# Optimization experiments

Hardware: AMD Instinct MI355X
Metric: run time of the kernel (lower is better)

Reference implementation:

```python
import jax, jax.numpy as jnp
import numpy as np

SPARSITY = 0.5


def get_subnet(s, sparsity):
    # edge-popup GetSubnet: binary mask keeping top (1-sparsity) fraction by value,
    # straight-through gradient (identity) in backward.
    flat = s.ravel()
    j = int(sparsity * flat.size)
    idx = jnp.argsort(flat)  # ascending
    mask = jnp.zeros_like(flat).at[idx[j:]].set(1.0).reshape(s.shape)
    return s + jax.lax.stop_gradient(mask - s)


def setup_inputs() -> dict:
    key = jax.random.key(0)
    k1, k2, k3, k4, k5 = jax.random.split(key, 5)
    B, F, R, O = 4096, 2048, 8, 2048
    return {
        "x": jax.random.normal(k1, (B, F), dtype=jnp.float32),
        "weight1": jax.random.normal(k2, (R, F), dtype=jnp.float32),
        "weight2": jax.random.normal(k3, (O, F * R), dtype=jnp.float32),
        "scores1": jax.random.normal(k4, (R, F), dtype=jnp.float32),
        "scores2": jax.random.normal(k5, (O, F * R), dtype=jnp.float32),
    }


def reference(x, weight1, weight2, scores1, scores2):
    B = x.shape[0]
    # masked weight1, broadcast-multiply repeated input
    w1 = weight1 * get_subnet(jnp.abs(scores1), SPARSITY)        # [R, F]
    h = x[:, None, :] * w1[None, :, :]                           # [B, R, F]
    h = jax.nn.relu(h)
    # permute(0,2,1).reshape -> feature-major flattening [B, F*R]
    h = jnp.transpose(h, (0, 2, 1)).reshape(B, -1)
    # masked weight2, dense GEMM
    w2 = weight2 * get_subnet(jnp.abs(scores2), SPARSITY)        # [O, F*R]
    return h @ w2.T                                              # [B, O]
```

## Files before the change

### kernel.cpp

```cpp
#include <hip/hip_runtime.h>
#include <stdint.h>

#define B_ 4096
#define F_ 2048
#define R_ 8
#define O_ 2048
#define N2 (O_ * F_ * R_)
#define N1 (R_ * F_)
#define K2SEL ((uint32_t)(N2 / 2))
#define K1SEL ((uint32_t)(N1 / 2))
#define TIE_CAP 8192


__device__ __forceinline__ uint32_t fkey(float s) {
    return __float_as_uint(fabsf(s));
}
__device__ __forceinline__ ushort f2bf(float f) {
    uint32_t u = __float_as_uint(f);
    return (ushort)((u + 0x7FFFu + ((u >> 16) & 1u)) >> 16);
}
__device__ __forceinline__ float bf2f(ushort h) {
    return __uint_as_float(((uint32_t)h) << 16);
}

__global__ void init_kernel(uint32_t* w) {
    int t = threadIdx.x;
    for (int i = t; i < 2048; i += 256) w[64 + i] = 0;
    if (t == 0) {
        w[0] = 0; w[1] = K2SEL;
        w[2] = 0; w[3] = K1SEL;
        w[4] = 0; w[5] = 0;
    }
}

__global__ void hist_kernel(const float* __restrict__ s, int n,
                            const uint32_t* __restrict__ state,
                            uint32_t* __restrict__ hist, int pass) {
    __shared__ uint32_t h[256];
    for (int i = threadIdx.x; i < 256; i += blockDim.x) h[i] = 0;
    __syncthreads();

    uint32_t prefix = state[0];
    int shift_pref = 32 - 8 * pass;
    int shift_bin  = 24 - 8 * pass;

    int stride = gridDim.x * blockDim.x;
    int i0 = blockIdx.x * blockDim.x + threadIdx.x;
    const float4* s4 = reinterpret_cast<const float4*>(s);
    int n4 = n >> 2;
    for (int i = i0; i < n4; i += stride) {
        float4 v = s4[i];
        uint32_t b[4] = { fkey(v.x), fkey(v.y), fkey(v.z), fkey(v.w) };
        if (pass == 0) {
            #pragma unroll
            for (int e = 0; e < 4; ++e) atomicAdd(&h[b[e] >> 24], 1u);
        } else {
            #pragma unroll
            for (int e = 0; e < 4; ++e)
                if ((b[e] >> shift_pref) == prefix)
                    atomicAdd(&h[(b[e] >> shift_bin) & 255u], 1u);
        }
    }
    __syncthreads();
    for (int i = threadIdx.x; i < 256; i += blockDim.x)
        if (h[i]) atomicAdd(&hist[i], h[i]);
}

__global__ void scan_kernel(uint32_t* state, const uint32_t* hist) {
    if (threadIdx.x == 0 && blockIdx.x == 0) {
        uint32_t K = state[1];
        uint32_t prefix = state[0];
        uint32_t cum = 0;
        for (int b = 255; b >= 0; --b) {
            uint32_t hb = hist[b];
            if (cum + hb >= K) {
                state[0] = (prefix << 8) | (uint32_t)b;
                state[1] = K - cum;
                break;
            }
            cum += hb;
        }
    }
}

__global__ void tie_kernel(const float* __restrict__ s, int n,
                           const uint32_t* __restrict__ state,
                           uint32_t* __restrict__ count, uint32_t* __restrict__ list) {
    uint32_t target = state[0];
    int stride = gridDim.x * blockDim.x;
    int i0 = blockIdx.x * blockDim.x + threadIdx.x;
    const float4* s4 = reinterpret_cast<const float4*>(s);
    int n4 = n >> 2;
    for (int i = i0; i < n4; i += stride) {
        float4 v = s4[i];
        uint32_t b[4] = { fkey(v.x), fkey(v.y), fkey(v.z), fkey(v.w) };
        #pragma unroll
        for (int e = 0; e < 4; ++e) {
            if (b[e] == target) {
                uint32_t p = atomicAdd(count, 1u);
                if (p < TIE_CAP) list[p] = (uint32_t)(4 * i + e);
            }
        }
    }
}

__global__ void cutoff_kernel(const uint32_t* __restrict__ count,
                              const uint32_t* __restrict__ list,
                              const uint32_t* __restrict__ state,
                              uint32_t* __restrict__ T, int n) {
    __shared__ uint32_t cnt;
    uint32_t c = *count; if (c > TIE_CAP) c = TIE_CAP;
    uint32_t n1 = state[1];
    uint32_t lo = 0, hi = (uint32_t)(n - 1);
    while (lo < hi) {
        uint32_t mid = lo + (hi - lo + 1) / 2;
        if (threadIdx.x == 0) cnt = 0;
        __syncthreads();
        uint32_t local = 0;
        for (uint32_t i = threadIdx.x; i < c; i += blockDim.x)
            if (list[i] >= mid) local++;
        if (local) atomicAdd(&cnt, local);
        __syncthreads();
        uint32_t cv = cnt;
        __syncthreads();
        if (cv >= n1) lo = mid; else hi = mid - 1;
    }
    if (threadIdx.x == 0) { T[0] = lo; T[1] = state[0]; }
}

__global__ void w1t_kernel(const float* __restrict__ w1, const float* __restrict__ s1,
                           const uint32_t* __restrict__ T1,
                           float* __restrict__ w1pt, float* __restrict__ w1nt) {
    int t = blockIdx.x * blockDim.x + threadIdx.x;
    if (t >= N1) return;
    uint32_t tb = T1[1], tc = T1[0];
    int r = t / F_, f = t - r * F_;
    uint32_t kb = fkey(s1[t]);
    bool m = (kb > tb) || (kb == tb && (uint32_t)t >= tc);
    float v = m ? w1[t] : 0.0f;
    w1pt[f * R_ + r] = fmaxf(v, 0.0f);
    w1nt[f * R_ + r] = fminf(v, 0.0f);
}

__global__ void xsplit_kernel(const float* __restrict__ x,
                              ushort* __restrict__ ph, ushort* __restrict__ pl,
                              ushort* __restrict__ nh, ushort* __restrict__ nl) {
    int t = blockIdx.x * blockDim.x + threadIdx.x;
    float4 v = reinterpret_cast<const float4*>(x)[t];
    float vv[4] = { v.x, v.y, v.z, v.w };
    ushort oph[4], opl[4], onh[4], onl[4];
    #pragma unroll
    for (int e = 0; e < 4; ++e) {
        float p = fmaxf(vv[e], 0.f), n = fminf(vv[e], 0.f);
        ushort h1 = f2bf(p); oph[e] = h1; opl[e] = f2bf(p - bf2f(h1));
        ushort h2 = f2bf(n); onh[e] = h2; onl[e] = f2bf(n - bf2f(h2));
    }
    *reinterpret_cast<ushort4*>(&ph[t * 4]) = make_ushort4(oph[0], oph[1], oph[2], oph[3]);
    *reinterpret_cast<ushort4*>(&pl[t * 4]) = make_ushort4(opl[0], opl[1], opl[2], opl[3]);
    *reinterpret_cast<ushort4*>(&nh[t * 4]) = make_ushort4(onh[0], onh[1], onh[2], onh[3]);
    *reinterpret_cast<ushort4*>(&nl[t * 4]) = make_ushort4(onl[0], onl[1], onl[2], onl[3]);
}

__global__ void wbuild_kernel(const float* __restrict__ w2, const float* __restrict__ s2,
                              const uint32_t* __restrict__ T2,
                              const float* __restrict__ w1pt, const float* __restrict__ w1nt,
                              ushort* __restrict__ bph, ushort* __restrict__ bpl,
                              ushort* __restrict__ bnh, ushort* __restrict__ bnl) {
    int t = blockIdx.x * blockDim.x + threadIdx.x;
    int f = t & (F_ - 1);
    uint32_t tb = T2[1], tc = T2[0];
    int base = (t >> 11) * (F_ * R_) + f * R_;

    float4 wa = *reinterpret_cast<const float4*>(w2 + base);
    float4 wb = *reinterpret_cast<const float4*>(w2 + base + 4);
    float4 sa = *reinterpret_cast<const float4*>(s2 + base);
    float4 sb = *reinterpret_cast<const float4*>(s2 + base + 4);
    float4 pa = *reinterpret_cast<const float4*>(w1pt + f * R_);
    float4 pb = *reinterpret_cast<const float4*>(w1pt + f * R_ + 4);
    float4 na = *reinterpret_cast<const float4*>(w1nt + f * R_);
    float4 nb = *reinterpret_cast<const float4*>(w1nt + f * R_ + 4);

    float wv[8] = { wa.x, wa.y, wa.z, wa.w, wb.x, wb.y, wb.z, wb.w };
    float sv[8] = { sa.x, sa.y, sa.z, sa.w, sb.x, sb.y, sb.z, sb.w };
    float pv[8] = { pa.x, pa.y, pa.z, pa.w, pb.x, pb.y, pb.z, pb.w };
    float nv[8] = { na.x, na.y, na.z, na.w, nb.x, nb.y, nb.z, nb.w };

    float accp = 0.f, accn = 0.f;
    #pragma unroll
    for (int r = 0; r < 8; ++r) {
        uint32_t kb = fkey(sv[r]);
        bool m = (kb > tb) || (kb == tb && (uint32_t)(base + r) >= tc);
        float wm = m ? wv[r] : 0.0f;
        accp = fmaf(pv[r], wm, accp);
        accn = fmaf(nv[r], wm, accn);
    }
    ushort h1 = f2bf(accp); bph[t] = h1; bpl[t] = f2bf(accp - bf2f(h1));
    ushort h2 = f2bf(accn); bnh[t] = h2; bnl[t] = f2bf(accn - bf2f(h2));
}

typedef __attribute__((ext_vector_type(8))) short bf16x8;
typedef __attribute__((ext_vector_type(4))) float f32x4;

__device__ __forceinline__ void gload16(const void* g, void* l) {
    __builtin_amdgcn_global_load_lds((const __attribute__((address_space(1))) void*)g,
                                     (__attribute__((address_space(3))) void*)l, 16, 0, 0);
}

__global__ __launch_bounds__(256) void mfma_gemm(
    const ushort* __restrict__ aph, const ushort* __restrict__ apl,
    const ushort* __restrict__ anh, const ushort* __restrict__ anl,
    const ushort* __restrict__ bph, const ushort* __restrict__ bpl,
    const ushort* __restrict__ bnh, const ushort* __restrict__ bnl,
    float* __restrict__ out) {
    __shared__ ushort lds[4][128][32];

    const int tid  = threadIdx.x;
    const int wid  = tid >> 6;
    const int lane = tid & 63;
    const int brow = blockIdx.y * 128;
    const int bcol = blockIdx.x * 128;
    const int wr = (wid >> 1) * 64;
    const int wc = (wid & 1) * 64;

    f32x4 acc[4][4] = {};

    const int srow = lane >> 2;
    const int scol = (lane & 3) * 8;

    #pragma unroll 1
    for (int plane = 0; plane < 2; ++plane) {
        const ushort* tsrc =
            (wid == 0) ? (plane ? anh : aph) :
            (wid == 1) ? (plane ? anl : apl) :
            (wid == 2) ? (plane ? bnh : bph) :
                         (plane ? bnl : bpl);
        const int rowbase = (wid < 2) ? brow : bcol;

        #pragma unroll 1
        for (int k0 = 0; k0 < F_; k0 += 32) {
            #pragma unroll
            for (int t = 0; t < 8; ++t) {
                const ushort* g = tsrc + (size_t)(rowbase + t * 16 + srow) * F_ + k0 + scol;
                gload16(g, (void*)&lds[wid][t * 16][0]);
            }
            __syncthreads();

            bf16x8 ah[4], al[4], bh[4], bl[4];
            const int fr = lane & 15;
            const int kc = (lane >> 4) * 8;
            #pragma unroll
            for (int i = 0; i < 4; ++i) {
                ah[i] = *(const bf16x8*)&lds[0][wr + i * 16 + fr][kc];
                al[i] = *(const bf16x8*)&lds[1][wr + i * 16 + fr][kc];
                bh[i] = *(const bf16x8*)&lds[2][wc + i * 16 + fr][kc];
                bl[i] = *(const bf16x8*)&lds[3][wc + i * 16 + fr][kc];
            }
            #pragma unroll
            for (int i = 0; i < 4; ++i)
                #pragma unroll
                for (int j = 0; j < 4; ++j) {
                    acc[i][j] = __builtin_amdgcn_mfma_f32_16x16x32_bf16(ah[i], bh[j], acc[i][j], 0, 0, 0);
                    acc[i][j] = __builtin_amdgcn_mfma_f32_16x16x32_bf16(ah[i], bl[j], acc[i][j], 0, 0, 0);
                    acc[i][j] = __builtin_amdgcn_mfma_f32_16x16x32_bf16(al[i], bh[j], acc[i][j], 0, 0, 0);
                }
            __syncthreads();
        }
    }

    #pragma unroll
    for (int i = 0; i < 4; ++i) {
        int orow0 = brow + wr + i * 16 + (lane >> 4) * 4;
        #pragma unroll
        for (int j = 0; j < 4; ++j) {
            int ocol = bcol + wc + j * 16 + (lane & 15);
            #pragma unroll
            for (int q = 0; q < 4; ++q)
                out[(size_t)(orow0 + q) * O_ + ocol] = acc[i][j][q];
        }
    }
}

extern "C" void kernel_launch(void* const* d_in, const int* in_sizes, int n_in,
                              void* d_out, int out_size, void* d_ws, size_t ws_size,
                              hipStream_t stream) {
    const float* x  = (const float*)d_in[0];
    const float* w1 = (const float*)d_in[1];
    const float* w2 = (const float*)d_in[2];
    const float* s1 = (const float*)d_in[3];
    const float* s2 = (const float*)d_in[4];
    float* out = (float*)d_out;

    uint32_t* w = (uint32_t*)d_ws;
    uint32_t* state2 = w + 0;
    uint32_t* state1 = w + 2;
    uint32_t* cnt2 = w + 4;
    uint32_t* cnt1 = w + 5;
    uint32_t* T2 = w + 6;
    uint32_t* T1 = w + 8;
    uint32_t* hist2 = w + 64;
    uint32_t* hist1 = w + 1088;
    uint32_t* tie2 = w + 2112;
    uint32_t* tie1 = w + 2112 + TIE_CAP;

    float* w1pt = (float*)((char*)d_ws + 131072);
    float* w1nt = w1pt + N1;

    char* base = (char*)d_ws + 262144;
    ushort* aph = (ushort*)(base);
    ushort* apl = aph + (size_t)B_ * F_;
    ushort* anh = apl + (size_t)B_ * F_;
    ushort* anl = anh + (size_t)B_ * F_;
    ushort* bph = anl + (size_t)B_ * F_;
    ushort* bpl = bph + (size_t)O_ * F_;
    ushort* bnh = bpl + (size_t)O_ * F_;
    ushort* bnl = bnh + (size_t)O_ * F_;

    init_kernel<<<1, 256, 0, stream>>>(w);

    xsplit_kernel<<<(B_ * F_ / 4) / 256, 256, 0, stream>>>(x, aph, apl, anh, anl);

    for (int p = 0; p < 4; ++p) {
        hist_kernel<<<2048, 256, 0, stream>>>(s2, N2, state2, hist2 + p * 256, p);
        scan_kernel<<<1, 1, 0, stream>>>(state2, hist2 + p * 256);
    }
    tie_kernel<<<2048, 256, 0, stream>>>(s2, N2, state2, cnt2, tie2);
    cutoff_kernel<<<1, 256, 0, stream>>>(cnt2, tie2, state2, T2, N2);

    for (int p = 0; p < 4; ++p) {
        hist_kernel<<<64, 256, 0, stream>>>(s1, N1, state1, hist1 + p * 256, p);
        scan_kernel<<<1, 1, 0, stream>>>(state1, hist1 + p * 256);
    }
    tie_kernel<<<64, 256, 0, stream>>>(s1, N1, state1, cnt1, tie1);
    cutoff_kernel<<<1, 256, 0, stream>>>(cnt1, tie1, state1, T1, N1);

    w1t_kernel<<<N1 / 256, 256, 0, stream>>>(w1, s1, T1, w1pt, w1nt);

    wbuild_kernel<<<(O_ * F_) / 256, 256, 0, stream>>>(w2, s2, T2, w1pt, w1nt,
                                                       bph, bpl, bnh, bnl);

    mfma_gemm<<<dim3(O_ / 128, B_ / 128), 256, 0, stream>>>(
        aph, apl, anh, anl, bph, bpl, bnh, bnl, out);
}
```

Baseline: 886.8 us.

## Replace four-pass radix select with 16-bit histogram plus candidate compaction

The median-threshold selection over the 33M-element scores2 drops from four 8-bit histogram passes plus a tie pass to one pass building a 16-bit global histogram, replicated 16 ways to spread atomic contention. A second pass compacts candidates that share the chosen 16-bit prefix, and a single block finishes the remaining bits and tie-breaking from that list. The small scores1 selection is fused into one single-block kernel that works in shared memory and also writes the transposed w1 halves. This cuts full reads of scores2 from five to two and removes many small launches, at the cost of heavy global atomics on 1M bins and a fixed candidate cap that could overflow on skewed inputs.

Result: slower. 3.073 ms (+246.6%).

```diff
diff --git a/kernel.cpp b/kernel.cpp
--- a/kernel.cpp
+++ b/kernel.cpp
@@ -9,7 +9,8 @@
 #define N1 (R_ * F_)
 #define K2SEL ((uint32_t)(N2 / 2))
 #define K1SEL ((uint32_t)(N1 / 2))
-#define TIE_CAP 8192
+#define CAND_CAP (512 * 1024)
+#define TIE_CAP2 4096
 
 
 __device__ __forceinline__ uint32_t fkey(float s) {
@@ -23,123 +24,208 @@
     return __uint_as_float(((uint32_t)h) << 16);
 }
 
-__global__ void init_kernel(uint32_t* w) {
+__global__ void init_kernel(uint32_t* st, uint32_t* h16) {
+    int i0 = blockIdx.x * blockDim.x + threadIdx.x;
+    int stride = gridDim.x * blockDim.x;
+    for (int i = i0; i < 16 * 65536; i += stride) h16[i] = 0;
+    if (i0 == 0) st[4] = 0;
+}
+
+__global__ void hist16_kernel(const float* __restrict__ s, uint32_t* __restrict__ h16) {
+    int stride = gridDim.x * blockDim.x;
+    int i0 = blockIdx.x * blockDim.x + threadIdx.x;
+    uint32_t rep = ((uint32_t)blockIdx.x & 15u) << 16;
+    const float4* s4 = reinterpret_cast<const float4*>(s);
+    for (int i = i0; i < N2 / 4; i += stride) {
+        float4 v = s4[i];
+        atomicAdd(&h16[rep | (fkey(v.x) >> 16)], 1u);
+        atomicAdd(&h16[rep | (fkey(v.y) >> 16)], 1u);
+        atomicAdd(&h16[rep | (fkey(v.z) >> 16)], 1u);
+        atomicAdd(&h16[rep | (fkey(v.w) >> 16)], 1u);
+    }
+}
+
+__global__ void scan16_kernel(uint32_t* __restrict__ h16, uint32_t* __restrict__ st) {
+    __shared__ uint32_t csum[256];
     int t = threadIdx.x;
-    for (int i = t; i < 2048; i += 256) w[64 + i] = 0;
+    int base = t * 256;
+    uint32_t sum = 0;
+    for (int b = 0; b < 256; ++b) {
+        uint32_t tot = 0;
+        #pragma unroll
+        for (int r = 0; r < 16; ++r) tot += h16[(r << 16) + base + b];
+        h16[base + b] = tot;
+        sum += tot;
+    }
+    csum[t] = sum;
+    __syncthreads();
     if (t == 0) {
-        w[0] = 0; w[1] = K2SEL;
-        w[2] = 0; w[3] = K1SEL;
-        w[4] = 0; w[5] = 0;
-    }
-}
-
-__global__ void hist_kernel(const float* __restrict__ s, int n,
-                            const uint32_t* __restrict__ state,
-                            uint32_t* __restrict__ hist, int pass) {
-    __shared__ uint32_t h[256];
-    for (int i = threadIdx.x; i < 256; i += blockDim.x) h[i] = 0;
-    __syncthreads();
-
-    uint32_t prefix = state[0];
-    int shift_pref = 32 - 8 * pass;
-    int shift_bin  = 24 - 8 * pass;
-
+        uint32_t K = K2SEL, cum = 0;
+        int chunk = 255;
+        for (; chunk > 0; --chunk) {
+            if (cum + csum[chunk] >= K) break;
+            cum += csum[chunk];
+        }
+        for (int b = 255; b >= 0; --b) {
+            uint32_t tot = h16[chunk * 256 + b];
+            if (cum + tot >= K) { st[0] = (uint32_t)(chunk * 256 + b); st[1] = K - cum; break; }
+            cum += tot;
+        }
+    }
+}
+
+__global__ void compact_kernel(const float* __restrict__ s,
+                               const uint32_t* __restrict__ st,
+                               uint32_t* __restrict__ cnt,
+                               uint32_t* __restrict__ candk, uint32_t* __restrict__ candi) {
+    uint32_t pfx = st[0];
     int stride = gridDim.x * blockDim.x;
     int i0 = blockIdx.x * blockDim.x + threadIdx.x;
     const float4* s4 = reinterpret_cast<const float4*>(s);
-    int n4 = n >> 2;
-    for (int i = i0; i < n4; i += stride) {
-        float4 v = s4[i];
-        uint32_t b[4] = { fkey(v.x), fkey(v.y), fkey(v.z), fkey(v.w) };
-        if (pass == 0) {
-            #pragma unroll
-            for (int e = 0; e < 4; ++e) atomicAdd(&h[b[e] >> 24], 1u);
-        } else {
-            #pragma unroll
-            for (int e = 0; e < 4; ++e)
-                if ((b[e] >> shift_pref) == prefix)
-                    atomicAdd(&h[(b[e] >> shift_bin) & 255u], 1u);
-        }
-    }
-    __syncthreads();
-    for (int i = threadIdx.x; i < 256; i += blockDim.x)
-        if (h[i]) atomicAdd(&hist[i], h[i]);
-}
-
-__global__ void scan_kernel(uint32_t* state, const uint32_t* hist) {
-    if (threadIdx.x == 0 && blockIdx.x == 0) {
-        uint32_t K = state[1];
-        uint32_t prefix = state[0];
-        uint32_t cum = 0;
-        for (int b = 255; b >= 0; --b) {
-            uint32_t hb = hist[b];
-            if (cum + hb >= K) {
-                state[0] = (prefix << 8) | (uint32_t)b;
-                state[1] = K - cum;
-                break;
-            }
-            cum += hb;
-        }
-    }
-}
-
-__global__ void tie_kernel(const float* __restrict__ s, int n,
-                           const uint32_t* __restrict__ state,
-                           uint32_t* __restrict__ count, uint32_t* __restrict__ list) {
-    uint32_t target = state[0];
-    int stride = gridDim.x * blockDim.x;
-    int i0 = blockIdx.x * blockDim.x + threadIdx.x;
-    const float4* s4 = reinterpret_cast<const float4*>(s);
-    int n4 = n >> 2;
-    for (int i = i0; i < n4; i += stride) {
+    for (int i = i0; i < N2 / 4; i += stride) {
         float4 v = s4[i];
         uint32_t b[4] = { fkey(v.x), fkey(v.y), fkey(v.z), fkey(v.w) };
         #pragma unroll
         for (int e = 0; e < 4; ++e) {
-            if (b[e] == target) {
-                uint32_t p = atomicAdd(count, 1u);
-                if (p < TIE_CAP) list[p] = (uint32_t)(4 * i + e);
+            if ((b[e] >> 16) == pfx) {
+                uint32_t p = atomicAdd(cnt, 1u);
+                if (p < CAND_CAP) { candk[p] = b[e]; candi[p] = (uint32_t)(4 * i + e); }
             }
         }
     }
 }
 
-__global__ void cutoff_kernel(const uint32_t* __restrict__ count,
-                              const uint32_t* __restrict__ list,
-                              const uint32_t* __restrict__ state,
-                              uint32_t* __restrict__ T, int n) {
-    __shared__ uint32_t cnt;
-    uint32_t c = *count; if (c > TIE_CAP) c = TIE_CAP;
-    uint32_t n1 = state[1];
-    uint32_t lo = 0, hi = (uint32_t)(n - 1);
+__global__ void finish2_kernel(const uint32_t* __restrict__ candk,
+                               const uint32_t* __restrict__ candi,
+                               uint32_t* __restrict__ st) {
+    __shared__ uint32_t hist[256];
+    __shared__ uint32_t tie[TIE_CAP2];
+    __shared__ uint32_t sh[4];
+    int t = threadIdx.x;
+    uint32_t c = st[4]; if (c > CAND_CAP) c = CAND_CAP;
+    uint32_t prefix = st[0];
+    uint32_t K = st[1];
+
+    for (int p = 0; p < 2; ++p) {
+        int shift = 8 - 8 * p;
+        hist[t] = 0;
+        __syncthreads();
+        for (uint32_t i = t; i < c; i += 256) {
+            uint32_t k = candk[i];
+            if ((k >> (shift + 8)) == prefix) atomicAdd(&hist[(k >> shift) & 255u], 1u);
+        }
+        __syncthreads();
+        if (t == 0) {
+            uint32_t cum = 0;
+            for (int b = 255; b >= 0; --b) {
+                uint32_t hb = hist[b];
+                if (cum + hb >= K) { sh[2] = (uint32_t)b; sh[3] = K - cum; break; }
+                cum += hb;
+            }
+        }
+        __syncthreads();
+        prefix = (prefix << 8) | sh[2];
+        K = sh[3];
+        __syncthreads();
+    }
+    uint32_t T = prefix;
+
+    if (t == 0) sh[0] = 0;
+    __syncthreads();
+    for (uint32_t i = t; i < c; i += 256)
+        if (candk[i] == T) {
+            uint32_t p = atomicAdd(&sh[0], 1u);
+            if (p < TIE_CAP2) tie[p] = candi[i];
+        }
+    __syncthreads();
+    uint32_t tc = sh[0]; if (tc > TIE_CAP2) tc = TIE_CAP2;
+
+    uint32_t lo = 0, hi = (uint32_t)(N2 - 1);
     while (lo < hi) {
         uint32_t mid = lo + (hi - lo + 1) / 2;
-        if (threadIdx.x == 0) cnt = 0;
+        if (t == 0) sh[1] = 0;
         __syncthreads();
         uint32_t local = 0;
-        for (uint32_t i = threadIdx.x; i < c; i += blockDim.x)
-            if (list[i] >= mid) local++;
-        if (local) atomicAdd(&cnt, local);
-        __syncthreads();
-        uint32_t cv = cnt;
-        __syncthreads();
-        if (cv >= n1) lo = mid; else hi = mid - 1;
-    }
-    if (threadIdx.x == 0) { T[0] = lo; T[1] = state[0]; }
-}
-
-__global__ void w1t_kernel(const float* __restrict__ w1, const float* __restrict__ s1,
-                           const uint32_t* __restrict__ T1,
-                           float* __restrict__ w1pt, float* __restrict__ w1nt) {
-    int t = blockIdx.x * blockDim.x + threadIdx.x;
-    if (t >= N1) return;
-    uint32_t tb = T1[1], tc = T1[0];
-    int r = t / F_, f = t - r * F_;
-    uint32_t kb = fkey(s1[t]);
-    bool m = (kb > tb) || (kb == tb && (uint32_t)t >= tc);
-    float v = m ? w1[t] : 0.0f;
-    w1pt[f * R_ + r] = fmaxf(v, 0.0f);
-    w1nt[f * R_ + r] = fminf(v, 0.0f);
+        for (uint32_t i = t; i < tc; i += 256) if (tie[i] >= mid) local++;
+        if (local) atomicAdd(&sh[1], local);
+        __syncthreads();
+        uint32_t cv = sh[1];
+        __syncthreads();
+        if (cv >= K) lo = mid; else hi = mid - 1;
+    }
+    if (t == 0) { st[2] = lo; st[3] = T; }
+}
+
+__global__ void s1w1_kernel(const float* __restrict__ s1, const float* __restrict__ w1,
+                            float* __restrict__ w1pt, float* __restrict__ w1nt) {
+    __shared__ uint32_t keys[N1];
+    __shared__ uint32_t hist[256];
+    __shared__ uint32_t tie[1024];
+    __shared__ uint32_t sh[4];
+    int t = threadIdx.x;
+    for (int i = t; i < N1; i += 256) keys[i] = fkey(s1[i]);
+    __syncthreads();
+
+    uint32_t prefix = 0, K = K1SEL;
+    for (int p = 0; p < 4; ++p) {
+        int shift = 24 - 8 * p;
+        hist[t] = 0;
+        __syncthreads();
+        for (int i = t; i < N1; i += 256) {
+            uint32_t k = keys[i];
+            bool ok = (p == 0) || ((k >> (shift + 8)) == prefix);
+            if (ok) atomicAdd(&hist[(k >> shift) & 255u], 1u);
+        }
+        __syncthreads();
+        if (t == 0) {
+            uint32_t cum = 0;
+            for (int b = 255; b >= 0; --b) {
+                uint32_t hb = hist[b];
+                if (cum + hb >= K) { sh[2] = (uint32_t)b; sh[3] = K - cum; break; }
+                cum += hb;
+            }
+        }
+        __syncthreads();
+        prefix = (prefix << 8) | sh[2];
+        K = sh[3];
+        __syncthreads();
+    }
+    uint32_t T = prefix;
+
+    if (t == 0) sh[0] = 0;
+    __syncthreads();
+    for (int i = t; i < N1; i += 256)
+        if (keys[i] == T) {
+            uint32_t p = atomicAdd(&sh[0], 1u);
+            if (p < 1024) tie[p] = (uint32_t)i;
+        }
+    __syncthreads();
+    uint32_t tc = sh[0]; if (tc > 1024) tc = 1024;
+
+    uint32_t lo = 0, hi = (uint32_t)(N1 - 1);
+    while (lo < hi) {
+        uint32_t mid = lo + (hi - lo + 1) / 2;
+        if (t == 0) sh[1] = 0;
+        __syncthreads();
+        uint32_t local = 0;
+        for (uint32_t i = t; i < tc; i += 256) if (tie[i] >= mid) local++;
+        if (local) atomicAdd(&sh[1], local);
+        __syncthreads();
+        uint32_t cv = sh[1];
+        __syncthreads();
+        if (cv >= K) lo = mid; else hi = mid - 1;
+    }
+    __syncthreads();
+
+    for (int i = t; i < N1; i += 256) {
+        uint32_t k = keys[i];
+        bool m = (k > T) || (k == T && (uint32_t)i >= lo);
+        float v = m ? w1[i] : 0.0f;
+        int r = i >> 11;
+        int f = i & (F_ - 1);
+        w1pt[f * R_ + r] = fmaxf(v, 0.0f);
+        w1nt[f * R_ + r] = fminf(v, 0.0f);
+    }
 }
 
 __global__ void xsplit_kernel(const float* __restrict__ x,
@@ -290,23 +376,13 @@
     const float* s2 = (const float*)d_in[4];
     float* out = (float*)d_out;
 
-    uint32_t* w = (uint32_t*)d_ws;
-    uint32_t* state2 = w + 0;
-    uint32_t* state1 = w + 2;
-    uint32_t* cnt2 = w + 4;
-    uint32_t* cnt1 = w + 5;
-    uint32_t* T2 = w + 6;
-    uint32_t* T1 = w + 8;
-    uint32_t* hist2 = w + 64;
-    uint32_t* hist1 = w + 1088;
-    uint32_t* tie2 = w + 2112;
-    uint32_t* tie1 = w + 2112 + TIE_CAP;
-
-    float* w1pt = (float*)((char*)d_ws + 131072);
+    uint32_t* st = (uint32_t*)d_ws;
+
+    float* w1pt = (float*)((char*)d_ws + 4096);
     float* w1nt = w1pt + N1;
 
-    char* base = (char*)d_ws + 262144;
-    ushort* aph = (ushort*)(base);
+    char* baseA = (char*)d_ws + 262144;
+    ushort* aph = (ushort*)baseA;
     ushort* apl = aph + (size_t)B_ * F_;
     ushort* anh = apl + (size_t)B_ * F_;
     ushort* anl = anh + (size_t)B_ * F_;
@@ -315,27 +391,22 @@
     ushort* bnh = bpl + (size_t)O_ * F_;
     ushort* bnl = bnh + (size_t)O_ * F_;
 
-    init_kernel<<<1, 256, 0, stream>>>(w);
+    uint32_t* h16   = (uint32_t*)((char*)d_ws + 67371008);
+    uint32_t* candk = (uint32_t*)((char*)d_ws + 67371008 + (4u << 20));
+    uint32_t* candi = (uint32_t*)((char*)d_ws + 67371008 + (6u << 20));
+
+    init_kernel<<<1024, 256, 0, stream>>>(st, h16);
 
     xsplit_kernel<<<(B_ * F_ / 4) / 256, 256, 0, stream>>>(x, aph, apl, anh, anl);
 
-    for (int p = 0; p < 4; ++p) {
-        hist_kernel<<<2048, 256, 0, stream>>>(s2, N2, state2, hist2 + p * 256, p);
-        scan_kernel<<<1, 1, 0, stream>>>(state2, hist2 + p * 256);
-    }
-    tie_kernel<<<2048, 256, 0, stream>>>(s2, N2, state2, cnt2, tie2);
-    cutoff_kernel<<<1, 256, 0, stream>>>(cnt2, tie2, state2, T2, N2);
-
-    for (int p = 0; p < 4; ++p) {
-        hist_kernel<<<64, 256, 0, stream>>>(s1, N1, state1, hist1 + p * 256, p);
-        scan_kernel<<<1, 1, 0, stream>>>(state1, hist1 + p * 256);
-    }
-    tie_kernel<<<64, 256, 0, stream>>>(s1, N1, state1, cnt1, tie1);
-    cutoff_kernel<<<1, 256, 0, stream>>>(cnt1, tie1, state1, T1, N1);
-
-    w1t_kernel<<<N1 / 256, 256, 0, stream>>>(w1, s1, T1, w1pt, w1nt);
-
-    wbuild_kernel<<<(O_ * F_) / 256, 256, 0, stream>>>(w2, s2, T2, w1pt, w1nt,
+    hist16_kernel<<<2048, 256, 0, stream>>>(s2, h16);
+    scan16_kernel<<<1, 256, 0, stream>>>(h16, st);
+    compact_kernel<<<2048, 256, 0, stream>>>(s2, st, &st[4], candk, candi);
+    finish2_kernel<<<1, 256, 0, stream>>>(candk, candi, st);
+
+    s1w1_kernel<<<1, 256, 0, stream>>>(s1, w1, w1pt, w1nt);
+
+    wbuild_kernel<<<(O_ * F_) / 256, 256, 0, stream>>>(w2, s2, &st[2], w1pt, w1nt,
                                                        bph, bpl, bnh, bnl);
 
     mfma_gemm<<<dim3(O_ / 128, B_ / 128), 256, 0, stream>>>(
```
